# Performance work log

Measured on AMD Instinct MI355X. Metric: run time of the kernel, lower is better.

The kernel has to match this reference:

```python
import jax, jax.numpy as jnp
from jax import lax
import numpy as np

N = 131072
REG_STRENGTH = 0.1


def _pav_nonincreasing(y):
    """Pool-Adjacent-Violators: isotonic regression fit to y under a
    non-increasing constraint (L2 loss). Returns (solution, pool_idx, pool_size_per_elem).
    Classic O(n) stack algorithm expressed with lax.fori_loop / while_loop."""
    n = y.shape[0]
    means0 = jnp.zeros(n, y.dtype)   # pooled means stack
    counts0 = jnp.zeros(n, y.dtype)  # pool sizes stack

    def push(i, state):
        means, counts, top = state
        means = means.at[top].set(y[i])
        counts = counts.at[top].set(jnp.asarray(1.0, y.dtype))
        top = top + 1

        def cond(st):
            m, c, t = st
            # violation of non-increasing: later pool mean exceeds previous pool mean
            return (t > 1) & (m[t - 1] > m[t - 2])

        def merge(st):
            m, c, t = st
            ct = c[t - 1] + c[t - 2]
            mt = (m[t - 1] * c[t - 1] + m[t - 2] * c[t - 2]) / ct
            m = m.at[t - 2].set(mt)
            c = c.at[t - 2].set(ct)
            c = c.at[t - 1].set(jnp.asarray(0.0, y.dtype))
            return m, c, t - 1

        return lax.while_loop(cond, merge, (means, counts, top))

    means, counts, _top = lax.fori_loop(0, n, push, (means0, counts0, jnp.int32(0)))
    # expand pooled means back to element positions
    ends = jnp.cumsum(counts)  # pool end offsets (trailing entries saturate at n)
    pool_idx = jnp.searchsorted(ends, jnp.arange(n).astype(ends.dtype), side='right')
    return means[pool_idx], pool_idx, counts[pool_idx]


def isotonic_l2(y):
    sol, _, _ = _pav_nonincreasing(y)
    return sol


def soft_rank_1d(values, regularization_strength=REG_STRENGTH):
    """torchsort/fast-soft-sort soft_rank (ASCENDING, l2 regularization):
    projection of values/eps onto the permutahedron induced by w=[n..1]."""
    n = values.shape[0]
    z = values / jnp.asarray(regularization_strength, values.dtype)
    perm = jnp.argsort(-z)                 # descending sort permutation
    s = z[perm]
    w = jnp.arange(n, 0, -1, dtype=z.dtype)
    v = isotonic_l2(s - w)                 # dual solution via PAV
    primal = s - v                         # soft ranks in sorted order
    return jnp.zeros_like(primal).at[perm].set(primal)  # undo permutation


def setup_inputs() -> dict:
    key = jax.random.key(0)
    k1, k2 = jax.random.split(key)
    inp = jax.random.normal(k1, (N,), dtype=jnp.float32)
    tgt = jax.random.normal(k2, (N,), dtype=jnp.float32)
    return {"input": inp, "target": tgt}


def reference(input, target):
    ri = soft_rank_1d(input.ravel())
    rt = soft_rank_1d(target.ravel())
    ri0 = ri - jnp.mean(ri)
    rt0 = rt - jnp.mean(rt)
    loss = jnp.sum(ri0 * rt0) / (
        jnp.sqrt(jnp.sum(ri0 ** 2)) * jnp.sqrt(jnp.sum(rt0 ** 2))
    )
    return loss
```

## Files before the change

kernel.cpp:

```cpp
#include <hip/hip_runtime.h>
#include <math.h>

typedef unsigned int u32;
typedef unsigned long long u64;

#define N_ELEM 131072
#define NBIN 4096
#define NW4 (NBIN / 32)
#define XMIN (-5.5)
#define XSPAN 11.0
#define BINW (11.0 / 4096.0)
#define INVW ((float)(4096.0 / 11.0))
#define KRUN 31
#define CAP 160
#define GRID 128
#define BS 512
#define EPB 2048
#define NGRP 8
#define SCALE 1099511627776.0

#define ROOT_OFF (8 * 32)
#define DONE_OFF (9 * 32)
#define BAR_U32  (10 * 32)

__device__ __forceinline__ u32 cldu(const u32* p) {
  return __hip_atomic_load(p, __ATOMIC_RELAXED, __HIP_MEMORY_SCOPE_AGENT);
}
__device__ __forceinline__ u64 cldull(const u64* p) {
  return __hip_atomic_load(p, __ATOMIC_RELAXED, __HIP_MEMORY_SCOPE_AGENT);
}
__device__ __forceinline__ void cstd(double* p, double v) {
  __hip_atomic_store(p, v, __ATOMIC_RELAXED, __HIP_MEMORY_SCOPE_AGENT);
}
__device__ __forceinline__ double cldd(const double* p) {
  return __hip_atomic_load(p, __ATOMIC_RELAXED, __HIP_MEMORY_SCOPE_AGENT);
}

__device__ __forceinline__ int vbin(float x) {
  int b = (int)((x - (float)XMIN) * INVW);
  return b < 0 ? 0 : (b > NBIN - 1 ? NBIN - 1 : b);
}

__device__ __forceinline__ u64 shfl_up_u64(u64 v, int o) {
  u32 lo = (u32)v, hi = (u32)(v >> 32);
  lo = __shfl_up(lo, o);
  hi = __shfl_up(hi, o);
  return ((u64)hi << 32) | lo;
}

__device__ __forceinline__ void gbar(u32* bar) {
  __syncthreads();
  if (threadIdx.x == 0) {
    int g = (int)(blockIdx.x >> 4);
    u32 old = __hip_atomic_fetch_add(&bar[g * 32], 1u,
                                     __ATOMIC_RELAXED, __HIP_MEMORY_SCOPE_AGENT);
    if (old == 15u)
      __hip_atomic_fetch_add(&bar[ROOT_OFF], 1u,
                             __ATOMIC_RELAXED, __HIP_MEMORY_SCOPE_AGENT);
    while (__hip_atomic_load(&bar[ROOT_OFF], __ATOMIC_RELAXED,
                             __HIP_MEMORY_SCOPE_AGENT) < (u32)NGRP)
      __builtin_amdgcn_s_sleep(1);
  }
  __syncthreads();
}

__global__ __launch_bounds__(BS) void k_prep(
    const float* __restrict__ in0, const float* __restrict__ in1,
    u32* gbitsP, u32* bar, u32* gCnt, u64* gSum) {
  __shared__ u32 bits[NW4];
  const int blk = blockIdx.x, t = threadIdx.x;
  const int arr = blk >> 6, b = blk & 63;
  const float* pin = arr ? in1 : in0;
  if (t < NW4) bits[t] = 0u;
  __syncthreads();
  float4 v4 = ((const float4*)(pin + b * EPB))[t];
  float xs[4] = {v4.x, v4.y, v4.z, v4.w};
#pragma unroll
  for (int e = 0; e < 4; e++) {
    int bn = vbin(xs[e]);
    atomicOr(&bits[bn >> 5], 1u << (bn & 31));
  }
  __syncthreads();
  if (t < NW4) gbitsP[blk * NW4 + t] = bits[t];
  if (blk == 0 && t < BAR_U32) bar[t] = 0u;
  if (blk == 1 && t < 2 * CAP) gCnt[t] = 0u;
  if (blk == 2 && t < 2 * CAP) gSum[t] = 0ull;
}

__global__ __launch_bounds__(BS) void k_main(
    const float* __restrict__ in0, const float* __restrict__ in1,
    const u32* __restrict__ gbitsP, u32* bar, u32* gCnt, u64* gSum,
    double* part, float* out) {
  __shared__ struct {
    u32 bits[2 * NW4];
    u32 sc[CAP]; u64 ss[CAP];
    u32 h[CAP];
    u64 hs[CAP];
    float lv[2][CAP];
    double ls[2][CAP];
    int wtot[8];
    double s0[BS], s1[BS], s2[BS];
  } S;
  __shared__ int sh_ntop;
  __shared__ int sh_last;
  const int blk = blockIdx.x, t = threadIdx.x;
  const int arr = blk >> 6, b = blk & 63;
  const float* pin = arr ? in1 : in0;

  float4 v4 = ((const float4*)(pin + b * EPB))[t];
  float xs[4] = {v4.x, v4.y, v4.z, v4.w};

  if (t < 256) {
    int a2 = t >> 7, w = t & 127;
    int rbeg = a2 * 64, rend = rbeg + 64;
    u32 m = 0;
    for (int r = rbeg; r < rend; r++) m |= gbitsP[r * NW4 + w];
    S.bits[t] = m;
  }
  __syncthreads();

  int flag = 0;
  float tval = 0.f;
  if (t < 256) {
    int a2 = t >> 7, w = t & 127;
    u32 wt = S.bits[t];
    if (wt) {
      int b0 = __ffs((int)wt) - 1;
      int bin = w * 32 + b0;
      int prev = -1;
      if (w >= 1) {
        u32 x1 = S.bits[a2 * 128 + w - 1];
        if (x1) prev = (w - 1) * 32 + (31 - __clz(x1));
        else if (w >= 2) {
          u32 x2 = S.bits[a2 * 128 + w - 2];
          if (x2) prev = (w - 2) * 32 + (31 - __clz(x2));
        }
      }
      if (bin - prev - 1 >= KRUN) {
        flag = 1;
        tval = (float)(XMIN + ((double)bin - 0.5) * BINW);
      }
    }
  }
  {
    u64 bal = __ballot(flag != 0);
    int lane = t & 63, w_ = t >> 6;
    int rank = __popcll(bal & ((1ull << lane) - 1ull));
    if (lane == 0) S.wtot[w_] = __popcll(bal);
    __syncthreads();
    int m0 = S.wtot[0] + S.wtot[1];
    int m1 = S.wtot[2] + S.wtot[3];
    if (flag) {
      int a2 = t >> 7;
      int off = rank + ((w_ == 1) ? S.wtot[0] : 0) + ((w_ == 3) ? S.wtot[2] : 0);
      int m = a2 ? m1 : m0;
      int idx = m - off;
      if (idx >= 1 && idx <= CAP - 2) S.lv[a2][idx] = tval;
    }
    if (t == 0) {
      int c0 = m0 + 2; if (c0 > CAP) c0 = CAP;
      int c1 = m1 + 2; if (c1 > CAP) c1 = CAP;
      S.lv[0][0] = (float)(XMIN + XSPAN + 1.0);
      S.lv[0][c0 - 1] = (float)(XMIN - 1.0);
      S.lv[1][0] = (float)(XMIN + XSPAN + 1.0);
      S.lv[1][c1 - 1] = (float)(XMIN - 1.0);
      S.wtot[4] = c0; S.wtot[5] = c1;
    }
    __syncthreads();
  }
  int tcn[2] = {S.wtot[4], S.wtot[5]};

  {
    int cn = tcn[arr];
    for (int j = t; j < cn; j += BS) { S.sc[j] = 0u; S.ss[j] = 0ull; }
    __syncthreads();
    int lane = t & 63;
    for (int e = 0; e < 4; e++) {
      float x = xs[e];
      int lo = 0, hi = cn;
      while (lo < hi) {
        int mid = (lo + hi) >> 1;
        if (S.lv[arr][mid] >= x) lo = mid + 1; else hi = mid;
      }
      long long q = llrint((double)x * SCALE);
      u64 todo = ~0ull;
      while (todo) {
        int leader = (int)__ffsll(todo) - 1;
        int lo_l = __shfl(lo, leader);
        u64 grp = __ballot(lo == lo_l);
        long long vq = (lo == lo_l) ? q : 0ll;
        int vc = (lo == lo_l) ? 1 : 0;
#pragma unroll
        for (int o = 32; o > 0; o >>= 1) {
          vq += __shfl_xor(vq, o);
          vc += __shfl_xor(vc, o);
        }
        if (lane == leader) {
          atomicAdd(&S.sc[lo_l], (u32)vc);
          atomicAdd(&S.ss[lo_l], (u64)vq);
        }
        todo &= ~grp;
      }
    }
    __syncthreads();
    for (int j = t; j < cn; j += BS) {
      u32 c = S.sc[j];
      if (c) {
        atomicAdd(&gCnt[arr * CAP + j], c);
        atomicAdd(&gSum[arr * CAP + j], S.ss[j]);
      }
    }
  }
  gbar(bar);

  int segn[2];
  for (int a2 = 0; a2 < 2; a2++) {
    int cn = tcn[a2];
    for (int j = t; j < cn; j += BS) {
      S.h[j] = cldu(&gCnt[a2 * CAP + j]);
      S.hs[j] = cldull(&gSum[a2 * CAP + j]);
    }
    __syncthreads();
    if (t < 64) {
      int per = (cn + 63) >> 6;
      int beg = t * per, end = beg + per; if (end > cn) end = cn;
      u32 rc = 0; u64 rs = 0;
      for (int j = beg; j < end; j++) {
        rc += S.h[j]; rs += S.hs[j];
        S.h[j] = rc;  S.hs[j] = rs;
      }
      u32 tcv = rc; u64 tsv = rs;
      for (int o = 1; o < 64; o <<= 1) {
        u32 pc = __shfl_up(tcv, o);
        u64 ps = shfl_up_u64(tsv, o);
        if (t >= o) { tcv += pc; tsv += ps; }
      }
      u32 ec = tcv - rc; u64 es = tsv - rs;
      for (int j = beg; j < end; j++) { S.h[j] += ec; S.hs[j] += es; }
    }
    __syncthreads();
    double* Cv = (double*)S.hs;
    for (int j = t; j < cn; j += BS) {
      double pd = (double)S.h[j];
      double s = (double)(long long)S.hs[j] / SCALE;
      Cv[j] = s / 0.1 - (pd * (double)N_ELEM - pd * (pd - 1.0) * 0.5);
    }
    __syncthreads();
    if (t == 0) {
      int top = 0, aX = 0, bX = 0, prevP = -1;
      double cA = 0.0, cB = 0.0;
      for (int k = 0; k < cn; k++) {
        int i = (int)S.h[k];
        if (i == prevP) continue;
        prevP = i;
        double Ci = Cv[k];
        float vi = S.lv[a2][k];
        while (top >= 2) {
          double cr = (double)(bX - aX) * (Ci - cA) - (cB - cA) * (double)(i - aX);
          if (cr >= 0.0) {
            top--;
            bX = aX; cB = cA;
            if (top >= 2) { aX = (int)S.h[top - 2]; cA = Cv[top - 2]; }
          } else break;
        }
        S.h[top] = (u32)i; Cv[top] = Ci; S.lv[a2][top] = vi;
        aX = bX; cA = cB;
        bX = i;  cB = Ci;
        top++;
      }
      sh_ntop = top;
    }
    __syncthreads();
    {
      int top = sh_ntop;
      for (int k = t; k < top - 1; k += BS)
        S.ls[a2][k] = (Cv[k + 1] - Cv[k]) /
                      (double)((int)S.h[k + 1] - (int)S.h[k]);
      segn[a2] = top - 1;
    }
    __syncthreads();
  }

  {
    int n0 = segn[0], n1 = segn[1];
    const double m = 0.5 * (double)(N_ELEM + 1);
    double a0 = 0.0, a1 = 0.0, a2v = 0.0;
    float2 x2 = ((const float2*)(in0 + blk * 1024))[t];
    float2 y2 = ((const float2*)(in1 + blk * 1024))[t];
    float xx[2] = {x2.x, x2.y};
    float yy[2] = {y2.x, y2.y};
#pragma unroll
    for (int e = 0; e < 2; e++) {
      float x = xx[e], y = yy[e];
      int k0 = 0, k1 = 0;
      for (int k = 1; k < n0; k++) if (x <= S.lv[0][k]) k0 = k;
      for (int k = 1; k < n1; k++) if (y <= S.lv[1][k]) k1 = k;
      double ra = (double)x / 0.1 - S.ls[0][k0] - m;
      double rb = (double)y / 0.1 - S.ls[1][k1] - m;
      a0 += ra * rb;
      a1 += ra * ra;
      a2v += rb * rb;
    }
    S.s0[t] = a0; S.s1[t] = a1; S.s2[t] = a2v;
    __syncthreads();
    for (int off = BS / 2; off > 0; off >>= 1) {
      if (t < off) {
        S.s0[t] += S.s0[t + off];
        S.s1[t] += S.s1[t + off];
        S.s2[t] += S.s2[t + off];
      }
      __syncthreads();
    }
    if (t == 0) {
      cstd(&part[blk], S.s0[0]);
      cstd(&part[GRID + blk], S.s1[0]);
      cstd(&part[2 * GRID + blk], S.s2[0]);
    }
  }

  __syncthreads();
  if (t == 0) {
    u32 old = __hip_atomic_fetch_add(&bar[DONE_OFF], 1u,
                                     __ATOMIC_RELAXED, __HIP_MEMORY_SCOPE_AGENT);
    sh_last = (old == (u32)(GRID - 1)) ? 1 : 0;
  }
  __syncthreads();
  if (sh_last && t < 64) {
    double v0 = 0.0, v1 = 0.0, v2 = 0.0;
    for (int k = t; k < GRID; k += 64) {
      v0 += cldd(&part[k]);
      v1 += cldd(&part[GRID + k]);
      v2 += cldd(&part[2 * GRID + k]);
    }
#pragma unroll
    for (int off = 32; off > 0; off >>= 1) {
      v0 += __shfl_down(v0, off);
      v1 += __shfl_down(v1, off);
      v2 += __shfl_down(v2, off);
    }
    if (t == 0) out[0] = (float)(v0 / (sqrt(v1) * sqrt(v2)));
  }
}

extern "C" void kernel_launch(void* const* d_in, const int* in_sizes, int n_in,
                              void* d_out, int out_size, void* d_ws, size_t ws_size,
                              hipStream_t stream) {
  const float* in0 = (const float*)d_in[0];
  const float* in1 = (const float*)d_in[1];
  float* out = (float*)d_out;

  size_t off = 0;
  char* base = (char*)d_ws;
  auto alloc = [&](size_t bytes) -> char* {
    char* p = base + off;
    off += (bytes + 63) & ~(size_t)63;
    return p;
  };
  u32* gbitsP = (u32*)alloc(sizeof(u32) * GRID * NW4);
  u32* bar    = (u32*)alloc(sizeof(u32) * BAR_U32);
  u32* gCnt   = (u32*)alloc(sizeof(u32) * 2 * CAP);
  u64* gSum   = (u64*)alloc(sizeof(u64) * 2 * CAP);
  double* part = (double*)alloc(sizeof(double) * 3 * GRID);
  (void)ws_size; (void)in_sizes; (void)n_in; (void)out_size;

  k_prep<<<dim3(GRID), dim3(BS), 0, stream>>>(in0, in1, gbitsP, bar, gCnt, gSum);
  k_main<<<dim3(GRID), dim3(BS), 0, stream>>>(in0, in1, gbitsP, bar, gCnt, gSum,
                                              part, out);
}
```

Measured before the change: 34.88 us.

## Fuse prep and main kernels with an extra grid barrier and parallel per-array hull

Merges the bitmap prep kernel into the main kernel: per-block bin bitmaps are OR-reduced with global atomics into a single shared bitmap, followed by an extra software grid barrier, replacing a second kernel launch and a 64-row gather. Counters are zeroed in-kernel and the bitmap and barrier state are cleared with a memset. The prefix-sum and convex-hull stage now handles both arrays at once in two halves of the block instead of looping over them. A memset node is added to the stream, and the in-kernel zeroing of gCnt/gSum is not ordered against other blocks' atomics except through barrier 0.

```diff
diff --git a/kernel.cpp b/kernel.cpp
--- a/kernel.cpp
+++ b/kernel.cpp
@@ -17,17 +17,24 @@
 #define BS 512
 #define EPB 2048
 #define NGRP 8
+#define NBAR 2
 #define SCALE 1099511627776.0
 
-#define ROOT_OFF (8 * 32)
-#define DONE_OFF (9 * 32)
-#define BAR_U32  (10 * 32)
+#define ROOT_SLOT (NBAR * NGRP)
+#define DONE_OFF  ((NBAR * NGRP + NBAR) * 32)
+#define BAR_U32   ((NBAR * NGRP + NBAR + 1) * 32)
 
 __device__ __forceinline__ u32 cldu(const u32* p) {
   return __hip_atomic_load(p, __ATOMIC_RELAXED, __HIP_MEMORY_SCOPE_AGENT);
 }
+__device__ __forceinline__ void cstu(u32* p, u32 v) {
+  __hip_atomic_store(p, v, __ATOMIC_RELAXED, __HIP_MEMORY_SCOPE_AGENT);
+}
 __device__ __forceinline__ u64 cldull(const u64* p) {
   return __hip_atomic_load(p, __ATOMIC_RELAXED, __HIP_MEMORY_SCOPE_AGENT);
+}
+__device__ __forceinline__ void cstull(u64* p, u64 v) {
+  __hip_atomic_store(p, v, __ATOMIC_RELAXED, __HIP_MEMORY_SCOPE_AGENT);
 }
 __device__ __forceinline__ void cstd(double* p, double v) {
   __hip_atomic_store(p, v, __ATOMIC_RELAXED, __HIP_MEMORY_SCOPE_AGENT);
@@ -48,60 +55,37 @@
   return ((u64)hi << 32) | lo;
 }
 
-__device__ __forceinline__ void gbar(u32* bar) {
+__device__ __forceinline__ void gbar(u32* bar, int idx) {
   __syncthreads();
   if (threadIdx.x == 0) {
     int g = (int)(blockIdx.x >> 4);
-    u32 old = __hip_atomic_fetch_add(&bar[g * 32], 1u,
+    u32 old = __hip_atomic_fetch_add(&bar[(idx * NGRP + g) * 32], 1u,
                                      __ATOMIC_RELAXED, __HIP_MEMORY_SCOPE_AGENT);
     if (old == 15u)
-      __hip_atomic_fetch_add(&bar[ROOT_OFF], 1u,
+      __hip_atomic_fetch_add(&bar[(ROOT_SLOT + idx) * 32], 1u,
                              __ATOMIC_RELAXED, __HIP_MEMORY_SCOPE_AGENT);
-    while (__hip_atomic_load(&bar[ROOT_OFF], __ATOMIC_RELAXED,
+    while (__hip_atomic_load(&bar[(ROOT_SLOT + idx) * 32], __ATOMIC_RELAXED,
                              __HIP_MEMORY_SCOPE_AGENT) < (u32)NGRP)
       __builtin_amdgcn_s_sleep(1);
   }
   __syncthreads();
 }
 
-__global__ __launch_bounds__(BS) void k_prep(
+__global__ __launch_bounds__(BS) void k_mega(
     const float* __restrict__ in0, const float* __restrict__ in1,
-    u32* gbitsP, u32* bar, u32* gCnt, u64* gSum) {
-  __shared__ u32 bits[NW4];
-  const int blk = blockIdx.x, t = threadIdx.x;
-  const int arr = blk >> 6, b = blk & 63;
-  const float* pin = arr ? in1 : in0;
-  if (t < NW4) bits[t] = 0u;
-  __syncthreads();
-  float4 v4 = ((const float4*)(pin + b * EPB))[t];
-  float xs[4] = {v4.x, v4.y, v4.z, v4.w};
-#pragma unroll
-  for (int e = 0; e < 4; e++) {
-    int bn = vbin(xs[e]);
-    atomicOr(&bits[bn >> 5], 1u << (bn & 31));
-  }
-  __syncthreads();
-  if (t < NW4) gbitsP[blk * NW4 + t] = bits[t];
-  if (blk == 0 && t < BAR_U32) bar[t] = 0u;
-  if (blk == 1 && t < 2 * CAP) gCnt[t] = 0u;
-  if (blk == 2 && t < 2 * CAP) gSum[t] = 0ull;
-}
-
-__global__ __launch_bounds__(BS) void k_main(
-    const float* __restrict__ in0, const float* __restrict__ in1,
-    const u32* __restrict__ gbitsP, u32* bar, u32* gCnt, u64* gSum,
+    u32* gbits, u32* bar, u32* gCnt, u64* gSum,
     double* part, float* out) {
   __shared__ struct {
     u32 bits[2 * NW4];
     u32 sc[CAP]; u64 ss[CAP];
-    u32 h[CAP];
-    u64 hs[CAP];
+    u32 h[2][CAP];
+    u64 hs[2][CAP];
     float lv[2][CAP];
     double ls[2][CAP];
     int wtot[8];
+    int ntop[2];
     double s0[BS], s1[BS], s2[BS];
   } S;
-  __shared__ int sh_ntop;
   __shared__ int sh_last;
   const int blk = blockIdx.x, t = threadIdx.x;
   const int arr = blk >> 6, b = blk & 63;
@@ -110,43 +94,58 @@
   float4 v4 = ((const float4*)(pin + b * EPB))[t];
   float xs[4] = {v4.x, v4.y, v4.z, v4.w};
 
-  if (t < 256) {
+  if (t < NW4) S.bits[t] = 0u;
+  {
+    int i = blk * BS + t;
+    if (i < 2 * CAP) { cstu(&gCnt[i], 0u); cstull(&gSum[i], 0ull); }
+  }
+  __syncthreads();
+#pragma unroll
+  for (int e = 0; e < 4; e++) {
+    int bn = vbin(xs[e]);
+    atomicOr(&S.bits[bn >> 5], 1u << (bn & 31));
+  }
+  __syncthreads();
+  if (t < NW4) {
+    u32 w = S.bits[t];
+    if (w) atomicOr(&gbits[arr * NW4 + t], w);
+  }
+  gbar(bar, 0);
+
+  if (t < 2 * NW4) {
     int a2 = t >> 7, w = t & 127;
-    int rbeg = a2 * 64, rend = rbeg + 64;
-    u32 m = 0;
-    for (int r = rbeg; r < rend; r++) m |= gbitsP[r * NW4 + w];
-    S.bits[t] = m;
-  }
-  __syncthreads();
-
-  int flag = 0;
-  float tval = 0.f;
-  if (t < 256) {
-    int a2 = t >> 7, w = t & 127;
-    u32 wt = S.bits[t];
-    if (wt) {
-      int b0 = __ffs((int)wt) - 1;
-      int bin = w * 32 + b0;
-      int prev = -1;
-      if (w >= 1) {
-        u32 x1 = S.bits[a2 * 128 + w - 1];
-        if (x1) prev = (w - 1) * 32 + (31 - __clz(x1));
-        else if (w >= 2) {
-          u32 x2 = S.bits[a2 * 128 + w - 2];
-          if (x2) prev = (w - 2) * 32 + (31 - __clz(x2));
-        }
-      }
-      if (bin - prev - 1 >= KRUN) {
-        flag = 1;
-        tval = (float)(XMIN + ((double)bin - 0.5) * BINW);
-      }
-    }
-  }
-  {
+    S.bits[t] = cldu(&gbits[a2 * NW4 + w]);
+  }
+  __syncthreads();
+  {
+    int flag = 0;
+    float tval = 0.f;
+    if (t < 2 * NW4) {
+      int w = t & 127;
+      u32 wt = S.bits[t];
+      if (wt) {
+        int b0 = __ffs((int)wt) - 1;
+        int bin = w * 32 + b0;
+        int prev = -1;
+        int a2 = t >> 7;
+        if (w >= 1) {
+          u32 x1 = S.bits[a2 * 128 + w - 1];
+          if (x1) prev = (w - 1) * 32 + (31 - __clz(x1));
+          else if (w >= 2) {
+            u32 x2 = S.bits[a2 * 128 + w - 2];
+            if (x2) prev = (w - 2) * 32 + (31 - __clz(x2));
+          }
+        }
+        if (bin - prev - 1 >= KRUN) {
+          flag = 1;
+          tval = (float)(XMIN + ((double)bin - 0.5) * BINW);
+        }
+      }
+    }
     u64 bal = __ballot(flag != 0);
     int lane = t & 63, w_ = t >> 6;
     int rank = __popcll(bal & ((1ull << lane) - 1ull));
-    if (lane == 0) S.wtot[w_] = __popcll(bal);
+    if (lane == 0 && w_ < 8) S.wtot[w_] = __popcll(bal);
     __syncthreads();
     int m0 = S.wtot[0] + S.wtot[1];
     int m1 = S.wtot[2] + S.wtot[3];
@@ -168,10 +167,10 @@
     }
     __syncthreads();
   }
-  int tcn[2] = {S.wtot[4], S.wtot[5]};
-
-  {
-    int cn = tcn[arr];
+  const int tcn0 = S.wtot[4], tcn1 = S.wtot[5];
+
+  {
+    int cn = arr ? tcn1 : tcn0;
     for (int j = t; j < cn; j += BS) { S.sc[j] = 0u; S.ss[j] = 0ull; }
     __syncthreads();
     int lane = t & 63;
@@ -211,78 +210,77 @@
       }
     }
   }
-  gbar(bar);
-
-  int segn[2];
-  for (int a2 = 0; a2 < 2; a2++) {
-    int cn = tcn[a2];
-    for (int j = t; j < cn; j += BS) {
-      S.h[j] = cldu(&gCnt[a2 * CAP + j]);
-      S.hs[j] = cldull(&gSum[a2 * CAP + j]);
-    }
-    __syncthreads();
-    if (t < 64) {
+  gbar(bar, 1);
+
+  {
+    int half = t >> 8, ht = t & 255;
+    int cn = half ? tcn1 : tcn0;
+    for (int j = ht; j < cn; j += 256) {
+      S.h[half][j] = cldu(&gCnt[half * CAP + j]);
+      S.hs[half][j] = cldull(&gSum[half * CAP + j]);
+    }
+    __syncthreads();
+    if (ht < 64) {
       int per = (cn + 63) >> 6;
-      int beg = t * per, end = beg + per; if (end > cn) end = cn;
+      int beg = ht * per, end = beg + per; if (end > cn) end = cn;
       u32 rc = 0; u64 rs = 0;
       for (int j = beg; j < end; j++) {
-        rc += S.h[j]; rs += S.hs[j];
-        S.h[j] = rc;  S.hs[j] = rs;
+        rc += S.h[half][j]; rs += S.hs[half][j];
+        S.h[half][j] = rc;  S.hs[half][j] = rs;
       }
       u32 tcv = rc; u64 tsv = rs;
       for (int o = 1; o < 64; o <<= 1) {
         u32 pc = __shfl_up(tcv, o);
         u64 ps = shfl_up_u64(tsv, o);
-        if (t >= o) { tcv += pc; tsv += ps; }
+        if (ht >= o) { tcv += pc; tsv += ps; }
       }
       u32 ec = tcv - rc; u64 es = tsv - rs;
-      for (int j = beg; j < end; j++) { S.h[j] += ec; S.hs[j] += es; }
-    }
-    __syncthreads();
-    double* Cv = (double*)S.hs;
-    for (int j = t; j < cn; j += BS) {
-      double pd = (double)S.h[j];
-      double s = (double)(long long)S.hs[j] / SCALE;
+      for (int j = beg; j < end; j++) { S.h[half][j] += ec; S.hs[half][j] += es; }
+    }
+    __syncthreads();
+    double* Cv = (double*)S.hs[half];
+    for (int j = ht; j < cn; j += 256) {
+      double pd = (double)S.h[half][j];
+      double s = (double)(long long)S.hs[half][j] / SCALE;
       Cv[j] = s / 0.1 - (pd * (double)N_ELEM - pd * (pd - 1.0) * 0.5);
     }
     __syncthreads();
-    if (t == 0) {
+    if (ht == 0) {
       int top = 0, aX = 0, bX = 0, prevP = -1;
       double cA = 0.0, cB = 0.0;
       for (int k = 0; k < cn; k++) {
-        int i = (int)S.h[k];
+        int i = (int)S.h[half][k];
         if (i == prevP) continue;
         prevP = i;
         double Ci = Cv[k];
-        float vi = S.lv[a2][k];
+        float vi = S.lv[half][k];
         while (top >= 2) {
           double cr = (double)(bX - aX) * (Ci - cA) - (cB - cA) * (double)(i - aX);
           if (cr >= 0.0) {
             top--;
             bX = aX; cB = cA;
-            if (top >= 2) { aX = (int)S.h[top - 2]; cA = Cv[top - 2]; }
+            if (top >= 2) { aX = (int)S.h[half][top - 2]; cA = Cv[top - 2]; }
           } else break;
         }
-        S.h[top] = (u32)i; Cv[top] = Ci; S.lv[a2][top] = vi;
+        S.h[half][top] = (u32)i; Cv[top] = Ci; S.lv[half][top] = vi;
         aX = bX; cA = cB;
         bX = i;  cB = Ci;
         top++;
       }
-      sh_ntop = top;
+      S.ntop[half] = top;
     }
     __syncthreads();
     {
-      int top = sh_ntop;
-      for (int k = t; k < top - 1; k += BS)
-        S.ls[a2][k] = (Cv[k + 1] - Cv[k]) /
-                      (double)((int)S.h[k + 1] - (int)S.h[k]);
-      segn[a2] = top - 1;
-    }
-    __syncthreads();
-  }
-
-  {
-    int n0 = segn[0], n1 = segn[1];
+      int top = S.ntop[half];
+      for (int k = ht; k < top - 1; k += 256)
+        S.ls[half][k] = (Cv[k + 1] - Cv[k]) /
+                        (double)((int)S.h[half][k + 1] - (int)S.h[half][k]);
+    }
+    __syncthreads();
+  }
+
+  {
+    int n0 = S.ntop[0] - 1, n1 = S.ntop[1] - 1;
     const double m = 0.5 * (double)(N_ELEM + 1);
     double a0 = 0.0, a1 = 0.0, a2v = 0.0;
     float2 x2 = ((const float2*)(in0 + blk * 1024))[t];
@@ -356,14 +354,15 @@
     off += (bytes + 63) & ~(size_t)63;
     return p;
   };
-  u32* gbitsP = (u32*)alloc(sizeof(u32) * GRID * NW4);
-  u32* bar    = (u32*)alloc(sizeof(u32) * BAR_U32);
-  u32* gCnt   = (u32*)alloc(sizeof(u32) * 2 * CAP);
-  u64* gSum   = (u64*)alloc(sizeof(u64) * 2 * CAP);
+  u32* gbits = (u32*)alloc(sizeof(u32) * 2 * NW4);
+  u32* bar   = (u32*)alloc(sizeof(u32) * BAR_U32);
+  u32* gCnt  = (u32*)alloc(sizeof(u32) * 2 * CAP);
+  u64* gSum  = (u64*)alloc(sizeof(u64) * 2 * CAP);
   double* part = (double*)alloc(sizeof(double) * 3 * GRID);
   (void)ws_size; (void)in_sizes; (void)n_in; (void)out_size;
 
-  k_prep<<<dim3(GRID), dim3(BS), 0, stream>>>(in0, in1, gbitsP, bar, gCnt, gSum);
-  k_main<<<dim3(GRID), dim3(BS), 0, stream>>>(in0, in1, gbitsP, bar, gCnt, gSum,
-                                              part, out);
-}
+  hipMemsetAsync(gbits, 0, sizeof(u32) * (2 * NW4 + BAR_U32), stream);
+
+  k_mega<<<dim3(GRID), dim3(BS), 0, stream>>>(
+      in0, in1, gbits, bar, gCnt, gSum, part, out);
+}
```

New measurement: 27.93 us (median of 3 runs). 1.25x faster.
